# Optimization experiments

Hardware: AMD Instinct MI355X
Metric: run time of the kernel (lower is better)

Reference implementation:

```python
import jax, jax.numpy as jnp
import numpy as np


def setup_inputs() -> dict:
    key = jax.random.key(0)
    k1, k2 = jax.random.split(key)
    b, c, h, w = 16, 2048, 32, 32
    n_points = 64
    fea = jax.random.normal(k1, (b, c, h, w), dtype=jnp.float32)
    point_list = jax.random.uniform(k2, (n_points, 2), dtype=jnp.float32)  # (x, y) in [0,1)
    valid = jnp.ones((n_points,), dtype=bool)
    return {"fea": fea, "point_list": point_list, "valid": valid}


def reference(fea, point_list, valid):
    # forward_point of SimModel, with fea == backbone(x)['feat4']
    b, c, h, w = fea.shape
    # point_cur = [int(px*w), int(py*h)]  (points in [0,1) so trunc == floor)
    ix = jnp.clip((point_list[:, 0] * w).astype(jnp.int32), 0, w - 1)  # [P]
    iy = jnp.clip((point_list[:, 1] * h).astype(jnp.int32), 0, h - 1)  # [P]
    # gather query feature vectors at each point: [b, c, P]
    queries = fea[:, :, iy, ix]
    # cosine-normalize keys (over channel) and queries
    keys = fea / jnp.linalg.norm(fea, axis=1, keepdims=True)          # [b, c, h, w]
    q = queries / jnp.linalg.norm(queries, axis=1, keepdims=True)    # [b, c, P]
    # cosine-similarity attention over all h*w locations: [b, P, h*w]
    attn = jnp.einsum('bcp,bck->bpk', q, keys.reshape(b, c, h * w))
    # torch: attn = (attn - attn.min(-1)[0]) / attn.max(-1)[0]
    # (RHS fully evaluated first -> both min and max taken on the ORIGINAL attn)
    amin = attn.min(axis=-1, keepdims=True)
    amax = attn.max(axis=-1, keepdims=True)
    attn = (attn - amin) / amax
    soft_masks = attn.reshape(b, -1, h, w)                            # [b, P, h, w]
    # invalid points produce all-zero masks
    return jnp.where(valid[None, :, None, None], soft_masks, jnp.zeros((), soft_masks.dtype))
```

## Files before the change

kernel.cpp:

```cpp
#include <hip/hip_runtime.h>

#define BB 16
#define CC 2048
#define HH 32
#define WW 32
#define HW 1024
#define NP 64

#define PCH 32
#define NCH (CC/PCH)

#define KB 64
#define CT 64
#define CS 2
#define CHALF (CC/CS)
#define NSTEP (CHALF/CT)

typedef __bf16 bf16x8 __attribute__((ext_vector_type(8)));
typedef float  f32x4  __attribute__((ext_vector_type(4)));

__device__ __forceinline__ unsigned f2bf2(float lo, float hi) {
    unsigned a = __float_as_uint(lo);
    unsigned b = __float_as_uint(hi);
    a += 0x7fffu + ((a >> 16) & 1u);
    b += 0x7fffu + ((b >> 16) & 1u);
    return (a >> 16) | (b & 0xffff0000u);
}


__global__ __launch_bounds__(256) void prep_kernel(const float* __restrict__ fea,
                                                   const float* __restrict__ pl,
                                                   unsigned short* __restrict__ qbf,
                                                   float* __restrict__ np2) {
    int cch = blockIdx.x, b = blockIdx.y;
    int t = threadIdx.x, lane = t & 63, rr = t >> 6;

    int ix = (int)(pl[2 * lane + 0] * WW); ix = min(max(ix, 0), WW - 1);
    int iy = (int)(pl[2 * lane + 1] * HH); iy = min(max(iy, 0), HH - 1);
    int kp = iy * WW + ix;

    __shared__ unsigned short buf[2][4][HW];
    __shared__ unsigned short ex[NP][PCH + 4];

    float ssq[16];
#pragma unroll
    for (int i = 0; i < 16; ++i) ssq[i] = 0.f;

    const float* base = fea + ((size_t)b * CC + cch * PCH + rr) * HW + 4 * lane;

#pragma unroll
    for (int ph = 0; ph < PCH / 4; ++ph) {
        float4 fv[4];
#pragma unroll
        for (int s = 0; s < 4; ++s)
            fv[s] = *(const float4*)(base + (size_t)(ph * 4) * HW + 256 * s);
#pragma unroll
        for (int s = 0; s < 4; ++s) {
            ssq[4 * s + 0] += fv[s].x * fv[s].x;
            ssq[4 * s + 1] += fv[s].y * fv[s].y;
            ssq[4 * s + 2] += fv[s].z * fv[s].z;
            ssq[4 * s + 3] += fv[s].w * fv[s].w;
            uint2 pk;
            pk.x = f2bf2(fv[s].x, fv[s].y);
            pk.y = f2bf2(fv[s].z, fv[s].w);
            *(uint2*)&buf[ph & 1][rr][4 * lane + 256 * s] = pk;
        }
        __syncthreads();
        ex[lane][ph * 4 + rr] = buf[ph & 1][rr][kp];
    }
    __syncthreads();

    float* red = (float*)buf;
#pragma unroll
    for (int s = 0; s < 4; ++s) {
        f32x4 v = {ssq[4 * s + 0], ssq[4 * s + 1], ssq[4 * s + 2], ssq[4 * s + 3]};
        *(f32x4*)&red[rr * HW + 4 * lane + 256 * s] = v;
    }
    __syncthreads();
    {
        int k0 = 4 * t;
        f32x4 r0 = *(f32x4*)&red[0 * HW + k0];
        f32x4 r1 = *(f32x4*)&red[1 * HW + k0];
        f32x4 r2 = *(f32x4*)&red[2 * HW + k0];
        f32x4 r3 = *(f32x4*)&red[3 * HW + k0];
        f32x4 sum = (r0 + r1) + (r2 + r3);
        *(f32x4*)&np2[((size_t)cch * BB + b) * HW + k0] = sum;
    }
    {
        int p = t >> 2, part = t & 3;
        uint2 lo = *(uint2*)&ex[p][8 * part];
        uint2 hi = *(uint2*)&ex[p][8 * part + 4];
        uint4 o = make_uint4(lo.x, lo.y, hi.x, hi.y);
        *(uint4*)&qbf[((size_t)b * NP + p) * CC + cch * PCH + 8 * part] = o;
    }
}

__global__ __launch_bounds__(128) void nred_kernel(const float* __restrict__ np2,
                                                   float* __restrict__ rn) {
    int b = blockIdx.y;
    int k = blockIdx.x * 128 + threadIdx.x;
    float s = 0.f;
#pragma unroll 8
    for (int cch = 0; cch < NCH; ++cch)
        s += np2[((size_t)cch * BB + b) * HW + k];
    rn[(size_t)b * HW + k] = rsqrtf(s);
}

__global__ __launch_bounds__(256) void gemm_kernel(const float* __restrict__ fea,
                                                   const unsigned short* __restrict__ qbf,
                                                   float* __restrict__ dotp) {
    int id = blockIdx.x + (int)gridDim.x * blockIdx.y;
    int sid = (id & 7) * 64 + (id >> 3);
    int kc = sid & 15, cs = (sid >> 4) & 1, b = sid >> 5;

    int t = threadIdx.x, lane = t & 63, w = t >> 6;
    int gi = lane >> 4, ii = lane & 15;
    int k0 = KB * kc;
    int c0 = cs * CHALF;

    __shared__ __align__(16) unsigned short bt[2][CT][KB];

    int sc = t >> 2, sq = t & 3;
    const float* gsrc = fea + ((size_t)b * CC + c0 + sc) * HW + k0 + 4 * sq;

    const unsigned short* qb = qbf + (size_t)b * NP * CC + c0;

    f32x4 acc[4];
#pragma unroll
    for (int pt = 0; pt < 4; ++pt) acc[pt] = (f32x4){0.f, 0.f, 0.f, 0.f};

    union UA { int4 i; bf16x8 v; };

    float4 g[4];
#pragma unroll
    for (int h = 0; h < 4; ++h) g[h] = *(const float4*)(gsrc + 16 * h);

    int kb2 = 4 * w + (ii >> 2);
    int klo = ii & 3;

    for (int s = 0; s < NSTEP; ++s) {
        int cur = s & 1;
#pragma unroll
        for (int h = 0; h < 4; ++h) {
            int sw = ((4 * h + sq) ^ (sc & 15)) & 15;
            uint2 pk;
            pk.x = f2bf2(g[h].x, g[h].y);
            pk.y = f2bf2(g[h].z, g[h].w);
            *(uint2*)&bt[cur][sc][sw * 4] = pk;
        }
        __syncthreads();

        int sn = (s + 1 < NSTEP) ? s + 1 : s;
#pragma unroll
        for (int h = 0; h < 4; ++h)
            g[h] = *(const float4*)(gsrc + (size_t)sn * CT * HW + 16 * h);

#pragma unroll
        for (int cw = 0; cw < 2; ++cw) {
            union { unsigned short u[8]; bf16x8 v; } bf;
            int swb = kb2 ^ (8 * (gi & 1));
#pragma unroll
            for (int e = 0; e < 8; ++e) {
                int c = cw * 32 + 8 * gi + e;
                int sw = (swb ^ e) & 15;
                bf.u[e] = bt[cur][c][sw * 4 + klo];
            }
#pragma unroll
            for (int pt = 0; pt < 4; ++pt) {
                UA a;
                a.i = *(const int4*)(qb + (size_t)(16 * pt + ii) * CC
                                     + s * CT + cw * 32 + 8 * gi);
                acc[pt] = __builtin_amdgcn_mfma_f32_16x16x32_bf16(a.v, bf.v, acc[pt], 0, 0, 0);
            }
        }
        __syncthreads();
    }

    float* dbase = dotp + (((size_t)cs * BB + b) * NP) * HW;
#pragma unroll
    for (int pt = 0; pt < 4; ++pt) {
#pragma unroll
        for (int r = 0; r < 4; ++r) {
            int p = 16 * pt + 4 * gi + r;
            dbase[(size_t)p * HW + k0 + 16 * w + ii] = acc[pt][r];
        }
    }
}

__global__ __launch_bounds__(256) void finalize_kernel(const float* __restrict__ dotp,
                                                       const float* __restrict__ rn,
                                                       const float* __restrict__ pl,
                                                       const int* __restrict__ valid,
                                                       float* __restrict__ out) {
    int p = blockIdx.x, b = blockIdx.y;
    int t = threadIdx.x;
    int k0 = 4 * t;

    int ix = (int)(pl[2 * p + 0] * WW); ix = min(max(ix, 0), WW - 1);
    int iy = (int)(pl[2 * p + 1] * HH); iy = min(max(iy, 0), HH - 1);
    int kp = iy * WW + ix;
    float rnp = rn[(size_t)b * HW + kp];

    const float* d0p = dotp + (((size_t)0 * BB + b) * NP + p) * HW;
    const float* d1p = dotp + (((size_t)1 * BB + b) * NP + p) * HW;
    float4 d0 = *(const float4*)(d0p + k0);
    float4 d1 = *(const float4*)(d1p + k0);
    float4 rk = *(const float4*)&rn[(size_t)b * HW + k0];

    float val[4];
    val[0] = (d0.x + d1.x) * rk.x * rnp;
    val[1] = (d0.y + d1.y) * rk.y * rnp;
    val[2] = (d0.z + d1.z) * rk.z * rnp;
    val[3] = (d0.w + d1.w) * rk.w * rnp;

    float mn = fminf(fminf(val[0], val[1]), fminf(val[2], val[3]));
    float mx = fmaxf(fmaxf(val[0], val[1]), fmaxf(val[2], val[3]));
#pragma unroll
    for (int off = 32; off; off >>= 1) {
        mn = fminf(mn, __shfl_xor(mn, off));
        mx = fmaxf(mx, __shfl_xor(mx, off));
    }
    __shared__ float smn[4], smx[4];
    int wave = t >> 6;
    if ((t & 63) == 0) { smn[wave] = mn; smx[wave] = mx; }
    __syncthreads();
    mn = fminf(fminf(smn[0], smn[1]), fminf(smn[2], smn[3]));
    mx = fmaxf(fmaxf(smx[0], smx[1]), fmaxf(smx[2], smx[3]));

    bool vld = valid[p] != 0;
    float4 o;
    o.x = vld ? (val[0] - mn) / mx : 0.f;
    o.y = vld ? (val[1] - mn) / mx : 0.f;
    o.z = vld ? (val[2] - mn) / mx : 0.f;
    o.w = vld ? (val[3] - mn) / mx : 0.f;
    *(float4*)&out[((size_t)b * NP + p) * HW + k0] = o;
}

extern "C" void kernel_launch(void* const* d_in, const int* in_sizes, int n_in,
                              void* d_out, int out_size, void* d_ws, size_t ws_size,
                              hipStream_t stream) {
    const float* fea = (const float*)d_in[0];
    const float* pl  = (const float*)d_in[1];
    const int* valid = (const int*)d_in[2];
    float* out = (float*)d_out;

    unsigned short* qbf = (unsigned short*)d_ws;
    float* np2 = (float*)(qbf + (size_t)BB * NP * CC);
    float* rn  = np2 + (size_t)NCH * BB * HW;
    float* dotp = rn + (size_t)BB * HW;

    prep_kernel<<<dim3(NCH, BB), 256, 0, stream>>>(fea, pl, qbf, np2);
    nred_kernel<<<dim3(8, BB), 128, 0, stream>>>(np2, rn);
    gemm_kernel<<<dim3(16 * CS, BB), 256, 0, stream>>>(fea, qbf, dotp);
    finalize_kernel<<<dim3(NP, BB), 256, 0, stream>>>(dotp, rn, pl, valid, out);
}
```

Before: 73.29 us.

## Switch GEMM to 32x32x16 MFMA tiles with padded LDS and one barrier per step

The GEMM kernel now uses 32x32x16 bf16 MFMA, giving each wave a 32-point by 32-position output tile instead of four 16x16 tiles. The swizzled LDS layout is replaced by a row padding of 68 elements, and the global load pattern is changed so each thread stores contiguous 16-element chunks. The second __syncthreads per step is removed and the double buffer is relied on instead. The aim is fewer MFMA issues and less LDS-index arithmetic. The risks are LDS bank conflicts on the strided column reads and a possible race from dropping the trailing barrier.

Result: faster. 66.06 us (-9.9%).

```diff
diff --git a/kernel.cpp b/kernel.cpp
--- a/kernel.cpp
+++ b/kernel.cpp
@@ -15,9 +15,11 @@
 #define CS 2
 #define CHALF (CC/CS)
 #define NSTEP (CHALF/CT)
-
-typedef __bf16 bf16x8 __attribute__((ext_vector_type(8)));
-typedef float  f32x4  __attribute__((ext_vector_type(4)));
+#define BP 68
+
+typedef __bf16 bf16x8  __attribute__((ext_vector_type(8)));
+typedef float  f32x4   __attribute__((ext_vector_type(4)));
+typedef float  f32x16  __attribute__((ext_vector_type(16)));
 
 __device__ __forceinline__ unsigned f2bf2(float lo, float hi) {
     unsigned a = __float_as_uint(lo);
@@ -114,76 +116,59 @@
     int kc = sid & 15, cs = (sid >> 4) & 1, b = sid >> 5;
 
     int t = threadIdx.x, lane = t & 63, w = t >> 6;
-    int gi = lane >> 4, ii = lane & 15;
+    int pt = w >> 1, kt = w & 1;
+    int p0 = 32 * pt;
     int k0 = KB * kc;
     int c0 = cs * CHALF;
-
-    __shared__ __align__(16) unsigned short bt[2][CT][KB];
+    int lo = lane & 31, hi = lane >> 5;
+
+    __shared__ __align__(16) unsigned short bt[2][CT][BP];
 
     int sc = t >> 2, sq = t & 3;
-    const float* gsrc = fea + ((size_t)b * CC + c0 + sc) * HW + k0 + 4 * sq;
-
-    const unsigned short* qb = qbf + (size_t)b * NP * CC + c0;
-
-    f32x4 acc[4];
-#pragma unroll
-    for (int pt = 0; pt < 4; ++pt) acc[pt] = (f32x4){0.f, 0.f, 0.f, 0.f};
-
+    const float* gsrc = fea + ((size_t)b * CC + c0 + sc) * HW + k0 + 16 * sq;
+
+    const unsigned short* qb = qbf + ((size_t)b * NP + p0 + lo) * CC + c0 + 8 * hi;
+
+    f32x16 acc = {};
     union UA { int4 i; bf16x8 v; };
 
     float4 g[4];
 #pragma unroll
-    for (int h = 0; h < 4; ++h) g[h] = *(const float4*)(gsrc + 16 * h);
-
-    int kb2 = 4 * w + (ii >> 2);
-    int klo = ii & 3;
+    for (int h = 0; h < 4; ++h) g[h] = *(const float4*)(gsrc + 4 * h);
 
     for (int s = 0; s < NSTEP; ++s) {
         int cur = s & 1;
 #pragma unroll
         for (int h = 0; h < 4; ++h) {
-            int sw = ((4 * h + sq) ^ (sc & 15)) & 15;
             uint2 pk;
             pk.x = f2bf2(g[h].x, g[h].y);
             pk.y = f2bf2(g[h].z, g[h].w);
-            *(uint2*)&bt[cur][sc][sw * 4] = pk;
+            *(uint2*)&bt[cur][sc][16 * sq + 4 * h] = pk;
         }
         __syncthreads();
 
         int sn = (s + 1 < NSTEP) ? s + 1 : s;
 #pragma unroll
         for (int h = 0; h < 4; ++h)
-            g[h] = *(const float4*)(gsrc + (size_t)sn * CT * HW + 16 * h);
-
-#pragma unroll
-        for (int cw = 0; cw < 2; ++cw) {
+            g[h] = *(const float4*)(gsrc + (size_t)sn * CT * HW + 4 * h);
+
+#pragma unroll
+        for (int cw = 0; cw < 4; ++cw) {
             union { unsigned short u[8]; bf16x8 v; } bf;
-            int swb = kb2 ^ (8 * (gi & 1));
-#pragma unroll
-            for (int e = 0; e < 8; ++e) {
-                int c = cw * 32 + 8 * gi + e;
-                int sw = (swb ^ e) & 15;
-                bf.u[e] = bt[cur][c][sw * 4 + klo];
-            }
-#pragma unroll
-            for (int pt = 0; pt < 4; ++pt) {
-                UA a;
-                a.i = *(const int4*)(qb + (size_t)(16 * pt + ii) * CC
-                                     + s * CT + cw * 32 + 8 * gi);
-                acc[pt] = __builtin_amdgcn_mfma_f32_16x16x32_bf16(a.v, bf.v, acc[pt], 0, 0, 0);
-            }
+#pragma unroll
+            for (int e = 0; e < 8; ++e)
+                bf.u[e] = bt[cur][16 * cw + 8 * hi + e][32 * kt + lo];
+            UA a;
+            a.i = *(const int4*)(qb + (size_t)s * CT + 16 * cw);
+            acc = __builtin_amdgcn_mfma_f32_32x32x16_bf16(a.v, bf.v, acc, 0, 0, 0);
         }
-        __syncthreads();
     }
 
     float* dbase = dotp + (((size_t)cs * BB + b) * NP) * HW;
 #pragma unroll
-    for (int pt = 0; pt < 4; ++pt) {
-#pragma unroll
-        for (int r = 0; r < 4; ++r) {
-            int p = 16 * pt + 4 * gi + r;
-            dbase[(size_t)p * HW + k0 + 16 * w + ii] = acc[pt][r];
-        }
+    for (int r = 0; r < 16; ++r) {
+        int p = p0 + (r & 3) + 8 * (r >> 2) + 4 * hi;
+        dbase[(size_t)p * HW + k0 + 32 * kt + lo] = acc[r];
     }
 }
 
```
